# Performance work log

Measured on AMD Instinct MI355X. Metric: run time of the kernel, lower is better.

Reference implementation:

```python
import jax, jax.numpy as jnp
import numpy as np

NC = 80
CONF = 0.25
IOU_T = 0.45
MAX_DET = 100
ATTN_RES = 14
NUM_BASE = 5
TOPK = 1024          # candidate pre-filter (EfficientNMS-style)
SCALE = 0.25         # spatial_scale of ROIAlign


def setup_inputs() -> dict:
    key = jax.random.key(0)
    k1, k2, k3, k4 = jax.random.split(key, 4)
    B, A = 4, 25200
    test = jax.random.uniform(k1, (B, A, 5 + NC), dtype=jnp.float32)
    # scale boxes to image coords: cx,cy in [0,608), w,h in [0,120)
    box_scale = jnp.concatenate([jnp.array([608., 608., 120., 120.], jnp.float32),
                                 jnp.ones(1 + NC, jnp.float32)])
    test = test * box_scale
    attn = jax.random.normal(k2, (B, A, NUM_BASE * ATTN_RES * ATTN_RES), dtype=jnp.float32)
    bases = jax.random.normal(k3, (B, NUM_BASE - 1, 160, 160), dtype=jnp.float32)
    sem = jax.random.normal(k4, (B, 1, 160, 160), dtype=jnp.float32)
    return {"test": test, "attn": attn, "bases": bases, "sem": sem}


def _iou_matrix(b):
    # b: [K,4] xyxy
    area = jnp.clip(b[:, 2] - b[:, 0], 0) * jnp.clip(b[:, 3] - b[:, 1], 0)
    lt = jnp.maximum(b[:, None, :2], b[None, :, :2])
    rb = jnp.minimum(b[:, None, 2:], b[None, :, 2:])
    wh = jnp.clip(rb - lt, 0)
    inter = wh[..., 0] * wh[..., 1]
    return inter / (area[:, None] + area[None, :] - inter + 1e-9)


def _nms_single(boxes, scores):
    # boxes [A,4], scores [A,NC]. Class-aware greedy NMS over top-K candidates.
    flat = scores.reshape(-1)
    flat = jnp.where(flat > CONF, flat, -jnp.inf)
    top_s, top_i = jax.lax.top_k(flat, TOPK)
    anchor = top_i // NC
    cls = top_i % NC
    cb = boxes[anchor]                                   # [K,4]
    sup = (_iou_matrix(cb) > IOU_T) & (cls[:, None] == cls[None, :])

    def step(valid, _):
        s = jnp.where(valid, top_s, -jnp.inf)
        j = jnp.argmax(s)
        ok = jnp.isfinite(s[j])
        nv = (valid & ~sup[j]).at[j].set(False)
        return jnp.where(ok, nv, valid), (j, ok)

    _, (sel, selok) = jax.lax.scan(step, jnp.isfinite(top_s), None, length=MAX_DET)
    dboxes = jnp.where(selok[:, None], cb[sel], 0.)
    dscores = jnp.where(selok, top_s[sel], 0.)
    dcls = jnp.where(selok, cls[sel], 0).astype(jnp.int32)
    didx = jnp.where(selok, anchor[sel], 0).astype(jnp.int32)
    return selok.sum().astype(jnp.int32), dboxes, dscores, dcls, didx


def _roi_align(feat, rois, bidx, oh, ow, scale):
    # feat [B,C,H,W], rois [N,4] xyxy (input coords), half_pixel transform,
    # avg mode, 1 sample/bin (adaptive ratio = 1 here since bins < 1 px).
    N = rois.shape[0]
    B, C, H, W = feat.shape
    x1 = rois[:, 0] * scale - 0.5
    y1 = rois[:, 1] * scale - 0.5
    x2 = rois[:, 2] * scale - 0.5
    y2 = rois[:, 3] * scale - 0.5
    ys = y1[:, None] + (jnp.arange(oh, dtype=feat.dtype) + 0.5) * ((y2 - y1) / oh)[:, None]
    xs = x1[:, None] + (jnp.arange(ow, dtype=feat.dtype) + 0.5) * ((x2 - x1) / ow)[:, None]

    def axis(coord, dim):
        valid = (coord > -1.0) & (coord < dim)
        c = jnp.clip(coord, 0.0, dim - 1.0)
        lo = jnp.floor(c)
        hi = jnp.clip(lo + 1, 0, dim - 1)
        return lo.astype(jnp.int32), hi.astype(jnp.int32), c - lo, valid

    y0, y1i, wy, vy = axis(ys, H)
    x0, x1i, wx, vx = axis(xs, W)
    featn = feat[bidx]                                   # [N,C,H,W]
    n = jnp.arange(N)[:, None, None]

    def g(Y, X):  # -> [N,oh,ow,C]
        return featn[n, :, Y[:, :, None], X[:, None, :]]

    wy_ = wy[:, :, None, None]
    wx_ = wx[:, None, :, None]
    val = (g(y0, x0) * (1 - wy_) * (1 - wx_) + g(y0, x1i) * (1 - wy_) * wx_
           + g(y1i, x0) * wy_ * (1 - wx_) + g(y1i, x1i) * wy_ * wx_)
    val = jnp.where((vy[:, :, None] & vx[:, None, :])[..., None], val, 0.)
    return jnp.transpose(val, (0, 3, 1, 2))                # [N,C,oh,ow]


def _forward(test, attn, bases_in, sem):
    bases = jnp.concatenate([bases_in, sem], axis=1)       # [B,5,H,W]
    conv = jnp.array([[1, 0, 1, 0], [0, 1, 0, 1],
                      [-0.5, 0, 0.5, 0], [0, -0.5, 0, 0.5]], test.dtype)
    boxes = test[:, :, :4] @ conv                          # cxcywh -> xyxy
    scores = test[:, :, 5:5 + NC] * test[:, :, 4:5]
    _, dboxes, dscores, dcls, didx = jax.vmap(_nms_single)(boxes, scores)
    B, P, H, W = bases.shape
    bidx = jnp.repeat(jnp.arange(B), MAX_DET)              # [B*D]
    box_i = didx.reshape(-1)
    sel_boxes = boxes[bidx, box_i]                         # [N,4]
    sel_masks = attn[bidx, box_i]                          # [N,980]
    pooled = _roi_align(bases, sel_boxes, bidx, H, W, SCALE)  # [N,5,H,W]
    coeffs = sel_masks.reshape(-1, NUM_BASE, ATTN_RES, ATTN_RES)
    coeffs = jax.image.resize(coeffs, (coeffs.shape[0], NUM_BASE, H, W), 'linear')
    coeffs = jax.nn.softmax(coeffs, axis=1)
    masks = jax.nn.sigmoid((pooled * coeffs).sum(axis=1).reshape(B, MAX_DET, H * W))
    return jnp.concatenate([dboxes, dscores[..., None],
                            dcls.astype(test.dtype)[..., None], masks], axis=-1)


def reference(test, attn, bases, sem):
    return _forward(test, attn, bases, sem)
```

## Files before the change

kernel.cpp:

```cpp
#include <hip/hip_runtime.h>
#include <stdint.h>

#define B_   4
#define A_   25200
#define NC_  80
#define ROW_ 85
#define ATT_ 980
#define MAXDET_ 100
#define TOPK_ 1024
#define CAP_  4096
#define OUTSTRIDE_ 25606
#define HW_ 160
#define HWHW_ 25600
#define CONF_ 0.25f
#define IOUT_ 0.45f

#define WS_HIST 0
#define WS_CNT  4096
#define WS_CAND 8192
#define WS_DETA 139264

typedef unsigned long long u64;
typedef unsigned u32;

__global__ void k_clear(char* w) {
    int i = blockIdx.x * 256 + threadIdx.x;
    if (i < 1028) ((u32*)w)[i] = 0u;
}

__global__ void k_hist(const float* __restrict__ test, char* __restrict__ w) {
    int b = blockIdx.y;
    __shared__ u32 h[256];
    if (threadIdx.x < 256) h[threadIdx.x] = 0u;
    __syncthreads();
    const int total = A_ * NC_;
    for (int e = blockIdx.x * 256 + threadIdx.x; e < total; e += 128 * 256) {
        u32 a = (u32)e / 80u;
        u32 c = (u32)e - a * 80u;
        const float* row = test + ((size_t)b * A_ + a) * ROW_;
        float s = row[5 + c] * row[4];
        if (s > CONF_) {
            u32 key = __float_as_uint(s);
            int wb = (int)(key >> 17) - 7936;
            wb = wb < 0 ? 0 : (wb > 255 ? 255 : wb);
            atomicAdd(&h[wb], 1u);
        }
    }
    __syncthreads();
    u32* hist = (u32*)(w + WS_HIST);
    if (threadIdx.x < 256 && h[threadIdx.x]) atomicAdd(&hist[b * 256 + threadIdx.x], h[threadIdx.x]);
}

__global__ void k_collect(const float* __restrict__ test, char* __restrict__ w) {
    int b = blockIdx.y;
    __shared__ u32 s[256];
    __shared__ int swtb;
    const u32* hist = (const u32*)(w + WS_HIST) + (size_t)b * 256;
    if (threadIdx.x < 256) s[threadIdx.x] = hist[threadIdx.x];
    if (threadIdx.x == 0) swtb = 0;
    __syncthreads();
    for (int off = 1; off < 256; off <<= 1) {
        u32 v = 0;
        if (threadIdx.x < 256) {
            v = s[threadIdx.x];
            if (threadIdx.x + off < 256) v += s[threadIdx.x + off];
        }
        __syncthreads();
        if (threadIdx.x < 256) s[threadIdx.x] = v;
        __syncthreads();
    }
    if (threadIdx.x < 256) {
        u32 Si = s[threadIdx.x];
        u32 Sn = (threadIdx.x == 255) ? 0u : s[threadIdx.x + 1];
        if (Si >= TOPK_ && Sn < TOPK_) swtb = threadIdx.x;
    }
    __syncthreads();
    int wtb = swtb;

    u32* cnt = (u32*)(w + WS_CNT);
    u64* cand = (u64*)(w + WS_CAND);
    const int total = A_ * NC_;
    for (int e = blockIdx.x * 256 + threadIdx.x; e < total; e += 128 * 256) {
        u32 a = (u32)e / 80u;
        u32 c = (u32)e - a * 80u;
        const float* row = test + ((size_t)b * A_ + a) * ROW_;
        float sc = row[5 + c] * row[4];
        if (sc > CONF_) {
            u32 key = __float_as_uint(sc);
            int wb = (int)(key >> 17) - 7936;
            wb = wb < 0 ? 0 : (wb > 255 ? 255 : wb);
            if (wb >= wtb) {
                u32 pos = atomicAdd(&cnt[b], 1u);
                if (pos < CAP_)
                    cand[(size_t)b * CAP_ + pos] = ((u64)key << 32) | (u64)(0xFFFFFFFFu - (u32)e);
            }
        }
    }
}

__device__ __forceinline__ bool sup_pair(float4 a, float4 b, int ca, int cbb) {
#pragma clang fp contract(off)
    if (ca != cbb) return false;
    float areaA = fmaxf(a.z - a.x, 0.f) * fmaxf(a.w - a.y, 0.f);
    float areaB = fmaxf(b.z - b.x, 0.f) * fmaxf(b.w - b.y, 0.f);
    float ltx = fmaxf(a.x, b.x), lty = fmaxf(a.y, b.y);
    float rbx = fminf(a.z, b.z), rby = fminf(a.w, b.w);
    float iw = fmaxf(rbx - ltx, 0.f), ih = fmaxf(rby - lty, 0.f);
    float inter = iw * ih;
    float iou = inter / (((areaA + areaB) - inter) + 1e-9f);
    return iou > IOUT_;
}

__global__ __launch_bounds__(1024) void k_sortnms(const float* __restrict__ test,
                                                  char* __restrict__ w,
                                                  float* __restrict__ out) {
    int b = blockIdx.x;
    int tid = threadIdx.x;
    __shared__ u64 sm[CAP_];
    __shared__ float4 cbs[TOPK_];
    __shared__ float tvs[TOPK_];
    __shared__ int tcs[TOPK_];
    __shared__ int tas[TOPK_];
    __shared__ u64 wmask[16];
    __shared__ int selA[MAXDET_];
    __shared__ u32 okA[MAXDET_];
    __shared__ int sj;

    u32 cnt = ((const u32*)(w + WS_CNT))[b];
    int n = cnt < CAP_ ? (int)cnt : CAP_;
    int n2 = 1024;
    while (n2 < n) n2 <<= 1;
    const u64* cand = (const u64*)(w + WS_CAND) + (size_t)b * CAP_;
    for (int i = tid; i < n2; i += 1024) sm[i] = (i < n) ? cand[i] : 0ull;
    __syncthreads();
    for (int k = 2; k <= n2; k <<= 1) {
        for (int j = k >> 1; j > 0; j >>= 1) {
            for (int t = tid; t < n2; t += 1024) {
                int ixj = t ^ j;
                if (ixj > t) {
                    u64 a = sm[t], c = sm[ixj];
                    bool desc = ((t & k) == 0);
                    if (desc ? (a < c) : (a > c)) { sm[t] = c; sm[ixj] = a; }
                }
            }
            __syncthreads();
        }
    }
    int ntop = n < TOPK_ ? n : TOPK_;
    {
        int i = tid;
        if (i < ntop) {
            u64 v = sm[i];
            u32 key = (u32)(v >> 32);
            u32 idx = 0xFFFFFFFFu - (u32)(v & 0xFFFFFFFFull);
            u32 anchor = idx / 80u;
            u32 cls = idx - anchor * 80u;
            const float* tr = test + ((size_t)b * A_ + anchor) * ROW_;
            float cx = tr[0], cy = tr[1], ww = tr[2], hh = tr[3];
            float4 box;
            box.x = cx - 0.5f * ww; box.y = cy - 0.5f * hh;
            box.z = cx + 0.5f * ww; box.w = cy + 0.5f * hh;
            tvs[i] = __uint_as_float(key);
            tas[i] = (int)anchor; tcs[i] = (int)cls; cbs[i] = box;
        } else {
            tvs[i] = 0.f; tas[i] = 0; tcs[i] = 0;
            cbs[i] = make_float4(0.f, 0.f, 0.f, 0.f);
        }
    }
    __syncthreads();

    bool valid = (tid < ntop);
    float4 myb = cbs[tid];
    int myc = tcs[tid];
    for (int k = 0; k < MAXDET_; ++k) {
        u64 bal = __ballot(valid);
        if ((tid & 63) == 0) wmask[tid >> 6] = bal;
        __syncthreads();
        if (tid == 0) {
            int j = -1;
            for (int wv = 15; wv >= 0; --wv) {
                u64 m = wmask[wv];
                if (m) j = (wv << 6) + (__ffsll(m) - 1);
            }
            sj = j;
            selA[k] = j < 0 ? 0 : j;
            okA[k] = j < 0 ? 0u : 1u;
        }
        __syncthreads();
        int j = sj;
        if (j >= 0 && valid) {
            if (tid == j || sup_pair(cbs[j], myb, tcs[j], myc)) valid = false;
        }
    }
    __syncthreads();

    int* deta = (int*)(w + WS_DETA);
    for (int k = tid; k < MAXDET_; k += 1024) {
        int ok = (int)okA[k], s = selA[k];
        float b0 = 0, b1 = 0, b2 = 0, b3 = 0, sc = 0; int cls_ = 0, anc = 0;
        if (ok) {
            float4 bb = cbs[s];
            b0 = bb.x; b1 = bb.y; b2 = bb.z; b3 = bb.w;
            sc = tvs[s]; cls_ = tcs[s]; anc = tas[s];
        }
        size_t o = ((size_t)(b * MAXDET_ + k)) * OUTSTRIDE_;
        out[o + 0] = b0; out[o + 1] = b1; out[o + 2] = b2; out[o + 3] = b3;
        out[o + 4] = sc; out[o + 5] = (float)cls_;
        deta[b * MAXDET_ + k] = anc;
    }
}

__global__ void k_mask(const float* __restrict__ test, const float* __restrict__ attn,
                       const float* __restrict__ bases, const float* __restrict__ sem,
                       const char* __restrict__ w, float* __restrict__ out) {
    int roi = blockIdx.x;
    int b = roi / MAXDET_;
    int anchor = ((const int*)(w + WS_DETA))[roi];
    const float* t = test + ((size_t)b * A_ + anchor) * ROW_;
    float cx = t[0], cy = t[1], ww = t[2], hh = t[3];
    float bx1 = cx - 0.5f * ww, by1 = cy - 0.5f * hh;
    float bx2 = cx + 0.5f * ww, by2 = cy + 0.5f * hh;
    float rx1 = bx1 * 0.25f - 0.5f, ry1 = by1 * 0.25f - 0.5f;
    float rx2 = bx2 * 0.25f - 0.5f, ry2 = by2 * 0.25f - 0.5f;
    float xstep = (rx2 - rx1) / 160.f, ystep = (ry2 - ry1) / 160.f;

    __shared__ float att[5 * 196];
    __shared__ float sxw[HW_], syw[HW_], rzw[HW_];
    __shared__ int sxlo[HW_], sxhi[HW_], sylo[HW_], syhi[HW_];
    __shared__ int sxv[HW_], syv[HW_], rzlo[HW_];

    const float* arow = attn + ((size_t)b * A_ + anchor) * ATT_;
    for (int i = threadIdx.x; i < ATT_; i += 256) att[i] = arow[i];
    if (threadIdx.x < HW_) {
        int i = threadIdx.x;
        float coord = rx1 + (i + 0.5f) * xstep;
        sxv[i] = (coord > -1.0f) && (coord < 160.0f);
        float c = fminf(fmaxf(coord, 0.f), 159.f);
        float lo = floorf(c);
        sxlo[i] = (int)lo; sxhi[i] = min((int)lo + 1, 159); sxw[i] = c - lo;
        coord = ry1 + (i + 0.5f) * ystep;
        syv[i] = (coord > -1.0f) && (coord < 160.0f);
        c = fminf(fmaxf(coord, 0.f), 159.f);
        lo = floorf(c);
        sylo[i] = (int)lo; syhi[i] = min((int)lo + 1, 159); syw[i] = c - lo;
        float f = (i + 0.5f) * (14.f / 160.f) - 0.5f;
        float rc = fminf(fmaxf(f, 0.f), 13.f);
        float rlo = floorf(rc);
        rzlo[i] = (int)rlo; rzw[i] = rc - rlo;
    }
    __syncthreads();

    const float* bp[5];
    bp[0] = bases + ((size_t)b * 4 + 0) * HWHW_;
    bp[1] = bases + ((size_t)b * 4 + 1) * HWHW_;
    bp[2] = bases + ((size_t)b * 4 + 2) * HWHW_;
    bp[3] = bases + ((size_t)b * 4 + 3) * HWHW_;
    bp[4] = sem + (size_t)b * HWHW_;

    size_t obase = (size_t)roi * OUTSTRIDE_ + 6;
    int pstart = blockIdx.y * (HWHW_ / 8);
    int pend = pstart + (HWHW_ / 8);
    for (int p = pstart + (int)threadIdx.x; p < pend; p += 256) {
        int y = p / HW_, x = p - y * HW_;
        int ylo = sylo[y], yhi = syhi[y]; float wy = syw[y];
        int xlo = sxlo[x], xhi = sxhi[x]; float wx = sxw[x];
        bool v = sxv[x] && syv[y];
        float w00 = (1.f - wy) * (1.f - wx), w01 = (1.f - wy) * wx;
        float w10 = wy * (1.f - wx), w11 = wy * wx;
        int i00 = ylo * HW_ + xlo, i01 = ylo * HW_ + xhi;
        int i10 = yhi * HW_ + xlo, i11 = yhi * HW_ + xhi;
        float pooled[5];
#pragma unroll
        for (int c5 = 0; c5 < 5; ++c5) {
            float g = bp[c5][i00] * w00 + bp[c5][i01] * w01 + bp[c5][i10] * w10 + bp[c5][i11] * w11;
            pooled[c5] = v ? g : 0.f;
        }
        int cylo = rzlo[y]; float cwy = rzw[y]; int cyhi = min(cylo + 1, 13);
        int cxlo = rzlo[x]; float cwx = rzw[x]; int cxhi = min(cxlo + 1, 13);
        float c00 = (1.f - cwy) * (1.f - cwx), c01 = (1.f - cwy) * cwx;
        float c10 = cwy * (1.f - cwx), c11 = cwy * cwx;
        int j00 = cylo * 14 + cxlo, j01 = cylo * 14 + cxhi;
        int j10 = cyhi * 14 + cxlo, j11 = cyhi * 14 + cxhi;
        float cf[5]; float m = -1e30f;
#pragma unroll
        for (int c5 = 0; c5 < 5; ++c5) {
            const float* ap = att + c5 * 196;
            float g = ap[j00] * c00 + ap[j01] * c01 + ap[j10] * c10 + ap[j11] * c11;
            cf[c5] = g; m = fmaxf(m, g);
        }
        float se = 0.f, dot = 0.f;
#pragma unroll
        for (int c5 = 0; c5 < 5; ++c5) {
            float e = __expf(cf[c5] - m);
            se += e; dot += pooled[c5] * e;
        }
        dot /= se;
        out[obase + p] = 1.f / (1.f + __expf(-dot));
    }
}

extern "C" void kernel_launch(void* const* d_in, const int* in_sizes, int n_in,
                              void* d_out, int out_size, void* d_ws, size_t ws_size,
                              hipStream_t stream) {
    const float* test = (const float*)d_in[0];
    const float* attn = (const float*)d_in[1];
    const float* bases = (const float*)d_in[2];
    const float* sem = (const float*)d_in[3];
    float* out = (float*)d_out;
    char* w = (char*)d_ws;

    k_clear<<<5, 256, 0, stream>>>(w);
    k_hist<<<dim3(128, B_), 256, 0, stream>>>(test, w);
    k_collect<<<dim3(128, B_), 256, 0, stream>>>(test, w);
    k_sortnms<<<B_, 1024, 0, stream>>>(test, w, out);
    k_mask<<<dim3(B_ * MAXDET_, 8), 256, 0, stream>>>(test, attn, bases, sem, w, out);
}
```

Baseline: 694.9 us.

## Refine histogram bins, register/shuffle bitonic sort, single-barrier NMS loop

The score histogram moves from 256 to 1024 finer bins, so fewer candidates pass the threshold and the candidate cap can drop to 2048. The bitonic sort now keeps two elements per thread in registers, using wave shuffles for small strides and LDS only for strides of 128 or more, which removes most shared-memory passes and barriers. The greedy NMS loop has every thread compute the argmax from double-buffered ballot masks, which drops the second barrier per step, and it exits early once no candidates remain. The risk is that more than 2048 candidates land above the threshold bin and get truncated.

```diff
diff --git a/kernel.cpp b/kernel.cpp
--- a/kernel.cpp
+++ b/kernel.cpp
@@ -8,7 +8,9 @@
 #define ATT_ 980
 #define MAXDET_ 100
 #define TOPK_ 1024
-#define CAP_  4096
+#define CAP_  2048
+#define NBIN_ 1024
+#define BINBASE_ 64000
 #define OUTSTRIDE_ 25606
 #define HW_ 160
 #define HWHW_ 25600
@@ -16,22 +18,22 @@
 #define IOUT_ 0.45f
 
 #define WS_HIST 0
-#define WS_CNT  4096
-#define WS_CAND 8192
-#define WS_DETA 139264
+#define WS_CNT  16384
+#define WS_CAND 16448
+#define WS_DETA 81984
 
 typedef unsigned long long u64;
 typedef unsigned u32;
 
 __global__ void k_clear(char* w) {
     int i = blockIdx.x * 256 + threadIdx.x;
-    if (i < 1028) ((u32*)w)[i] = 0u;
+    if (i < B_ * NBIN_ + 4) ((u32*)w)[i] = 0u;
 }
 
 __global__ void k_hist(const float* __restrict__ test, char* __restrict__ w) {
     int b = blockIdx.y;
-    __shared__ u32 h[256];
-    if (threadIdx.x < 256) h[threadIdx.x] = 0u;
+    __shared__ u32 h[NBIN_];
+    for (int i = threadIdx.x; i < NBIN_; i += 256) h[i] = 0u;
     __syncthreads();
     const int total = A_ * NC_;
     for (int e = blockIdx.x * 256 + threadIdx.x; e < total; e += 128 * 256) {
@@ -41,38 +43,47 @@
         float s = row[5 + c] * row[4];
         if (s > CONF_) {
             u32 key = __float_as_uint(s);
-            int wb = (int)(key >> 17) - 7936;
-            wb = wb < 0 ? 0 : (wb > 255 ? 255 : wb);
+            int wb = (int)(key >> 14) - BINBASE_;
+            wb = wb < 0 ? 0 : (wb > NBIN_ - 1 ? NBIN_ - 1 : wb);
             atomicAdd(&h[wb], 1u);
         }
     }
     __syncthreads();
     u32* hist = (u32*)(w + WS_HIST);
-    if (threadIdx.x < 256 && h[threadIdx.x]) atomicAdd(&hist[b * 256 + threadIdx.x], h[threadIdx.x]);
+    for (int i = threadIdx.x; i < NBIN_; i += 256)
+        if (h[i]) atomicAdd(&hist[b * NBIN_ + i], h[i]);
 }
 
 __global__ void k_collect(const float* __restrict__ test, char* __restrict__ w) {
     int b = blockIdx.y;
-    __shared__ u32 s[256];
+    int tid = threadIdx.x;
+    __shared__ u32 hb[NBIN_];
+    __shared__ u32 cs[256];
     __shared__ int swtb;
-    const u32* hist = (const u32*)(w + WS_HIST) + (size_t)b * 256;
-    if (threadIdx.x < 256) s[threadIdx.x] = hist[threadIdx.x];
-    if (threadIdx.x == 0) swtb = 0;
+    const u32* hist = (const u32*)(w + WS_HIST) + (size_t)b * NBIN_;
+    for (int i = tid; i < NBIN_; i += 256) hb[i] = hist[i];
+    if (tid == 0) swtb = 0;
+    __syncthreads();
+    u32 c0 = hb[4 * tid], c1 = hb[4 * tid + 1], c2 = hb[4 * tid + 2], c3 = hb[4 * tid + 3];
+    cs[tid] = c0 + c1 + c2 + c3;
     __syncthreads();
     for (int off = 1; off < 256; off <<= 1) {
-        u32 v = 0;
-        if (threadIdx.x < 256) {
-            v = s[threadIdx.x];
-            if (threadIdx.x + off < 256) v += s[threadIdx.x + off];
-        }
+        u32 v = cs[tid];
+        if (tid + off < 256) v += cs[tid + off];
         __syncthreads();
-        if (threadIdx.x < 256) s[threadIdx.x] = v;
+        cs[tid] = v;
         __syncthreads();
     }
-    if (threadIdx.x < 256) {
-        u32 Si = s[threadIdx.x];
-        u32 Sn = (threadIdx.x == 255) ? 0u : s[threadIdx.x + 1];
-        if (Si >= TOPK_ && Sn < TOPK_) swtb = threadIdx.x;
+    {
+        u32 tail = (tid < 255) ? cs[tid + 1] : 0u;
+        u32 s3 = tail + c3;
+        u32 s2 = s3 + c2;
+        u32 s1 = s2 + c1;
+        u32 s0 = s1 + c0;
+        if (s3 >= TOPK_ && tail < TOPK_) swtb = 4 * tid + 3;
+        if (s2 >= TOPK_ && s3 < TOPK_)  swtb = 4 * tid + 2;
+        if (s1 >= TOPK_ && s2 < TOPK_)  swtb = 4 * tid + 1;
+        if (s0 >= TOPK_ && s1 < TOPK_)  swtb = 4 * tid + 0;
     }
     __syncthreads();
     int wtb = swtb;
@@ -80,15 +91,15 @@
     u32* cnt = (u32*)(w + WS_CNT);
     u64* cand = (u64*)(w + WS_CAND);
     const int total = A_ * NC_;
-    for (int e = blockIdx.x * 256 + threadIdx.x; e < total; e += 128 * 256) {
+    for (int e = blockIdx.x * 256 + tid; e < total; e += 128 * 256) {
         u32 a = (u32)e / 80u;
         u32 c = (u32)e - a * 80u;
         const float* row = test + ((size_t)b * A_ + a) * ROW_;
         float sc = row[5 + c] * row[4];
         if (sc > CONF_) {
             u32 key = __float_as_uint(sc);
-            int wb = (int)(key >> 17) - 7936;
-            wb = wb < 0 ? 0 : (wb > 255 ? 255 : wb);
+            int wb = (int)(key >> 14) - BINBASE_;
+            wb = wb < 0 ? 0 : (wb > NBIN_ - 1 ? NBIN_ - 1 : wb);
             if (wb >= wtb) {
                 u32 pos = atomicAdd(&cnt[b], 1u);
                 if (pos < CAP_)
@@ -111,60 +122,90 @@
     return iou > IOUT_;
 }
 
+__device__ __forceinline__ u64 maxu(u64 a, u64 b) { return a > b ? a : b; }
+__device__ __forceinline__ u64 minu(u64 a, u64 b) { return a < b ? a : b; }
+__device__ __forceinline__ u64 shflx(u64 v, int m) {
+    int lo = __shfl_xor((int)(u32)v, m);
+    int hi = __shfl_xor((int)(v >> 32), m);
+    return ((u64)(u32)hi << 32) | (u32)lo;
+}
+
 __global__ __launch_bounds__(1024) void k_sortnms(const float* __restrict__ test,
                                                   char* __restrict__ w,
                                                   float* __restrict__ out) {
     int b = blockIdx.x;
     int tid = threadIdx.x;
-    __shared__ u64 sm[CAP_];
+    int lane = tid & 63, wv = tid >> 6;
+    int x1 = wv * 128 + lane, x2 = x1 + 64;
+
+    __shared__ u64 lds[CAP_];
     __shared__ float4 cbs[TOPK_];
     __shared__ float tvs[TOPK_];
     __shared__ int tcs[TOPK_];
     __shared__ int tas[TOPK_];
-    __shared__ u64 wmask[16];
+    __shared__ u64 wmask[2][16];
     __shared__ int selA[MAXDET_];
-    __shared__ u32 okA[MAXDET_];
-    __shared__ int sj;
+    __shared__ int okA[MAXDET_];
 
     u32 cnt = ((const u32*)(w + WS_CNT))[b];
     int n = cnt < CAP_ ? (int)cnt : CAP_;
-    int n2 = 1024;
-    while (n2 < n) n2 <<= 1;
     const u64* cand = (const u64*)(w + WS_CAND) + (size_t)b * CAP_;
-    for (int i = tid; i < n2; i += 1024) sm[i] = (i < n) ? cand[i] : 0ull;
-    __syncthreads();
-    for (int k = 2; k <= n2; k <<= 1) {
-        for (int j = k >> 1; j > 0; j >>= 1) {
-            for (int t = tid; t < n2; t += 1024) {
-                int ixj = t ^ j;
-                if (ixj > t) {
-                    u64 a = sm[t], c = sm[ixj];
-                    bool desc = ((t & k) == 0);
-                    if (desc ? (a < c) : (a > c)) { sm[t] = c; sm[ixj] = a; }
+    u64 v1 = (x1 < n) ? cand[x1] : 0ull;
+    u64 v2 = (x2 < n) ? cand[x2] : 0ull;
+
+    for (int k = 2; k <= CAP_; k <<= 1) {
+        for (int j = k >> 1; j >= 128; j >>= 1) {
+            __syncthreads();
+            lds[x1] = v1; lds[x2] = v2;
+            __syncthreads();
+            u64 u1 = lds[x1 ^ j], u2 = lds[x2 ^ j];
+            bool q1 = ((x1 & j) == 0) == ((x1 & k) == 0);
+            bool q2 = ((x2 & j) == 0) == ((x2 & k) == 0);
+            v1 = q1 ? maxu(v1, u1) : minu(v1, u1);
+            v2 = q2 ? maxu(v2, u2) : minu(v2, u2);
+        }
+        if (k >= 128) {
+            bool de = (x1 & k) == 0;
+            u64 a = de ? maxu(v1, v2) : minu(v1, v2);
+            u64 c = de ? minu(v1, v2) : maxu(v1, v2);
+            v1 = a; v2 = c;
+        }
+        for (int j = (k >> 1) < 32 ? (k >> 1) : 32; j >= 1; j >>= 1) {
+            u64 u1 = shflx(v1, j), u2 = shflx(v2, j);
+            bool lo = (lane & j) == 0;
+            bool q1 = lo == ((x1 & k) == 0);
+            bool q2 = lo == ((x2 & k) == 0);
+            v1 = q1 ? maxu(v1, u1) : minu(v1, u1);
+            v2 = q2 ? maxu(v2, u2) : minu(v2, u2);
+        }
+    }
+
+    int ntop = n < TOPK_ ? n : TOPK_;
+    {
+        u64 vv[2] = { v1, v2 };
+        int xx[2] = { x1, x2 };
+#pragma unroll
+        for (int r = 0; r < 2; ++r) {
+            int x = xx[r];
+            if (x < TOPK_) {
+                if (x < ntop) {
+                    u64 v = vv[r];
+                    u32 key = (u32)(v >> 32);
+                    u32 idx = 0xFFFFFFFFu - (u32)(v & 0xFFFFFFFFull);
+                    u32 anchor = idx / 80u;
+                    u32 cls = idx - anchor * 80u;
+                    const float* tr = test + ((size_t)b * A_ + anchor) * ROW_;
+                    float cx = tr[0], cy = tr[1], ww = tr[2], hh = tr[3];
+                    float4 box;
+                    box.x = cx - 0.5f * ww; box.y = cy - 0.5f * hh;
+                    box.z = cx + 0.5f * ww; box.w = cy + 0.5f * hh;
+                    tvs[x] = __uint_as_float(key);
+                    tas[x] = (int)anchor; tcs[x] = (int)cls; cbs[x] = box;
+                } else {
+                    tvs[x] = 0.f; tas[x] = 0; tcs[x] = 0;
+                    cbs[x] = make_float4(0.f, 0.f, 0.f, 0.f);
                 }
             }
-            __syncthreads();
-        }
-    }
-    int ntop = n < TOPK_ ? n : TOPK_;
-    {
-        int i = tid;
-        if (i < ntop) {
-            u64 v = sm[i];
-            u32 key = (u32)(v >> 32);
-            u32 idx = 0xFFFFFFFFu - (u32)(v & 0xFFFFFFFFull);
-            u32 anchor = idx / 80u;
-            u32 cls = idx - anchor * 80u;
-            const float* tr = test + ((size_t)b * A_ + anchor) * ROW_;
-            float cx = tr[0], cy = tr[1], ww = tr[2], hh = tr[3];
-            float4 box;
-            box.x = cx - 0.5f * ww; box.y = cy - 0.5f * hh;
-            box.z = cx + 0.5f * ww; box.w = cy + 0.5f * hh;
-            tvs[i] = __uint_as_float(key);
-            tas[i] = (int)anchor; tcs[i] = (int)cls; cbs[i] = box;
-        } else {
-            tvs[i] = 0.f; tas[i] = 0; tcs[i] = 0;
-            cbs[i] = make_float4(0.f, 0.f, 0.f, 0.f);
         }
     }
     __syncthreads();
@@ -172,31 +213,31 @@
     bool valid = (tid < ntop);
     float4 myb = cbs[tid];
     int myc = tcs[tid];
+    int par = 0;
     for (int k = 0; k < MAXDET_; ++k) {
         u64 bal = __ballot(valid);
-        if ((tid & 63) == 0) wmask[tid >> 6] = bal;
+        if (lane == 0) wmask[par][wv] = bal;
         __syncthreads();
-        if (tid == 0) {
-            int j = -1;
-            for (int wv = 15; wv >= 0; --wv) {
-                u64 m = wmask[wv];
-                if (m) j = (wv << 6) + (__ffsll(m) - 1);
-            }
-            sj = j;
-            selA[k] = j < 0 ? 0 : j;
-            okA[k] = j < 0 ? 0u : 1u;
-        }
-        __syncthreads();
-        int j = sj;
-        if (j >= 0 && valid) {
-            if (tid == j || sup_pair(cbs[j], myb, tcs[j], myc)) valid = false;
-        }
+        int j = -1;
+#pragma unroll
+        for (int q = 15; q >= 0; --q) {
+            u64 m = wmask[par][q];
+            if (m) j = (q << 6) + __ffsll(m) - 1;
+        }
+        if (j < 0) {
+            if (tid == 0)
+                for (int kk = k; kk < MAXDET_; ++kk) { selA[kk] = 0; okA[kk] = 0; }
+            break;
+        }
+        if (tid == 0) { selA[k] = j; okA[k] = 1; }
+        if (valid && (tid == j || sup_pair(cbs[j], myb, tcs[j], myc))) valid = false;
+        par ^= 1;
     }
     __syncthreads();
 
     int* deta = (int*)(w + WS_DETA);
     for (int k = tid; k < MAXDET_; k += 1024) {
-        int ok = (int)okA[k], s = selA[k];
+        int ok = okA[k], s = selA[k];
         float b0 = 0, b1 = 0, b2 = 0, b3 = 0, sc = 0; int cls_ = 0, anc = 0;
         if (ok) {
             float4 bb = cbs[s];
@@ -309,7 +350,7 @@
     float* out = (float*)d_out;
     char* w = (char*)d_ws;
 
-    k_clear<<<5, 256, 0, stream>>>(w);
+    k_clear<<<17, 256, 0, stream>>>(w);
     k_hist<<<dim3(128, B_), 256, 0, stream>>>(test, w);
     k_collect<<<dim3(128, B_), 256, 0, stream>>>(test, w);
     k_sortnms<<<B_, 1024, 0, stream>>>(test, w, out);
```

Result: slower. 721.3 us (+3.8%).
